# Performance work log

Hardware: AMD Instinct MI355X
Metric: run time of the kernel (lower is better)

## Reference

```python
import jax, jax.numpy as jnp
import numpy as np

N_ENT = 100000
N_USR = 50000
N_REL = 16
D = 64
E_KG = 1500000
E_CF = 1500000
N_LAYERS = 3
LEAKY_SLOPE = 0.01  # torch nn.LeakyReLU default


def setup_inputs() -> dict:
    key = jax.random.key(0)
    ks = jax.random.split(key, 14)
    inv = 1.0 / np.sqrt(D)
    return {
        "ent_user_embed": jax.random.normal(ks[0], (N_ENT + N_USR, D), jnp.float32) * inv,
        "rel_embed": jax.random.normal(ks[1], (N_REL, D), jnp.float32) * inv,
        "Wk_w": jax.random.normal(ks[2], (2 * D, D), jnp.float32) * (1.0 / np.sqrt(2 * D)),
        "Wk_b": jnp.zeros((D,), jnp.float32),
        "Wa_w": jax.random.normal(ks[3], (D, D), jnp.float32) * inv,
        "Wb_w": jax.random.normal(ks[4], (D, D), jnp.float32) * inv,
        "kg_h": jax.random.randint(ks[5], (E_KG,), 0, N_ENT, jnp.int32),
        "kg_t": jax.random.randint(ks[6], (E_KG,), 0, N_ENT, jnp.int32),
        "kg_r": jax.random.randint(ks[7], (E_KG,), 0, N_REL, jnp.int32),
        "ain_row": jax.random.randint(ks[8], (E_CF,), 0, N_ENT + N_USR, jnp.int32),
        "ain_col": jax.random.randint(ks[9], (E_CF,), 0, N_ENT + N_USR, jnp.int32),
        "ain_val": jax.random.uniform(ks[10], (E_CF,), jnp.float32) * (1.0 / 64.0),
        "user_ids": jax.random.randint(ks[11], (1024,), 0, N_USR, jnp.int32) + N_ENT,
        "item_ids": jax.random.randint(ks[12], (2048,), 0, N_ENT, jnp.int32),
        "n_entities": N_ENT,
        "n_users": N_USR,
    }


def reference(ent_user_embed, rel_embed, Wk_w, Wk_b, Wa_w, Wb_w,
              kg_h, kg_t, kg_r, ain_row, ain_col, ain_val,
              user_ids, item_ids, n_entities, n_users):
    # ---- update_attention: per-edge KG attention + sparse row-softmax ----
    h_e = ent_user_embed[kg_h]          # [E, D] gather
    t_e = ent_user_embed[kg_t]          # [E, D] gather
    r_e = rel_embed[kg_r]               # [E, D]
    trans = jnp.concatenate([t_e, h_e], axis=1) @ Wk_w + Wk_b  # W_k([t||h])
    logits = jnp.sum(trans * r_e, axis=1)                      # [E]
    logits = jnp.where(logits >= 0, logits, LEAKY_SLOPE * logits)
    row_max = jax.ops.segment_max(logits, kg_h, num_segments=n_entities)
    ex = jnp.exp(logits - row_max[kg_h])
    row_sum = jax.ops.segment_sum(ex, kg_h, num_segments=n_entities)
    attn = ex / row_sum[kg_h]           # sparse softmax over dim=1 (per head row)

    n_total = n_entities + n_users

    def spmm_kg(x):   # A_kg @ x, A_kg is [n_ent, n_ent] COO with attn values
        return jax.ops.segment_sum(attn[:, None] * x[kg_t], kg_h, num_segments=n_entities)

    def spmm_ain(x):  # A_in @ x, [n_total, n_total] COO
        return jax.ops.segment_sum(ain_val[:, None] * x[ain_col], ain_row, num_segments=n_total)

    def fusion_gate(kg_embed, ig_embed):
        g = jax.nn.sigmoid(kg_embed @ Wa_w + ig_embed @ Wb_w)
        return g * kg_embed + (1.0 - g) * ig_embed

    # ---- get_embeddings: L layers of dual propagation + gated fusion ----
    e_entities = ent_user_embed[:n_entities]
    e_users = ent_user_embed[n_entities:]
    user_sum = e_users
    item_sum = e_entities
    e_items_dual = e_entities
    e_users_curr = e_users
    e_entities_curr = e_entities
    for _ in range(N_LAYERS):
        e_items_kg = spmm_kg(e_entities_curr)
        ig_input = jnp.concatenate([e_items_dual, e_users_curr], axis=0)
        ig_output = spmm_ain(ig_input)
        e_items_collab = ig_output[:n_entities]
        e_users_new = ig_output[n_entities:]
        e_items_dual = fusion_gate(e_items_kg, e_items_collab)
        item_sum = item_sum + e_items_collab
        user_sum = user_sum + e_users_new
        e_users_curr = e_users_new
        e_entities_curr = e_items_kg
        # mess_dropout = [0,0,0] (eval mode): no-op
    all_embed = jnp.concatenate([item_sum, user_sum], axis=0)  # [n_total, D]

    # ---- calc_score ----
    return all_embed[user_ids] @ all_embed[item_ids].T  # [n_u, n_i]
```

## Files before the change

kernel.cpp:

```cpp
#include <hip/hip_runtime.h>
#include <math.h>

#define N_ENT 100000
#define N_USR 50000
#define N_TOT 150000
#define N_ROWS 250000
#define DD 64

#define SCAN_BLK 256
#define SCAN_ITEMS 1024

#define SORT_T 4096
#define BUK_SHIFT 8
#define NBUKU 977
#define LDSCAP 5120

typedef _Float16 half8 __attribute__((ext_vector_type(8)));
typedef _Float16 half4 __attribute__((ext_vector_type(4)));
typedef _Float16 h2v __attribute__((ext_vector_type(2)));
typedef float floatx4 __attribute__((ext_vector_type(4)));

__global__ void k_rel(const float* __restrict__ Wk_w, const float* __restrict__ Wk_b,
                      const float* __restrict__ rel, float* __restrict__ uvr) {
    int r = blockIdx.x;
    int k = threadIdx.x;
    const float* rv = rel + r * DD;
    const float* wrow = Wk_w + k * DD;
    float s = 0.f;
    for (int j = 0; j < DD; ++j) s += wrow[j] * rv[j];
    uvr[r * 132 + k] = s;
    if (k == 0) {
        float c = 0.f;
        for (int j = 0; j < DD; ++j) c += Wk_b[j] * rv[j];
        uvr[r * 132 + 128] = c;
    }
}

__global__ __launch_bounds__(256) void k_proj(const float* __restrict__ embed,
        const float* __restrict__ uvr, float* __restrict__ Puv) {
    __shared__ float suvr[64 * 32];
    for (int i = threadIdx.x; i < 64 * 32; i += 256) {
        int d = i >> 5, sub = i & 31;
        suvr[i] = uvr[(sub & 15) * 132 + (sub >> 4) * 64 + d];
    }
    __syncthreads();
    int rowi = threadIdx.x >> 5;
    int sub = threadIdx.x & 31;
    int row = blockIdx.x * 8 + rowi;
    if (row >= N_ENT) return;
    const float* er = embed + (size_t)row * DD;
    float s = 0.f;
    for (int d = 0; d < DD; ++d) s = fmaf(er[d], suvr[d * 32 + sub], s);
    Puv[(size_t)row * 32 + sub] = s;
}

__global__ __launch_bounds__(256) void k_sort_hist(const int* __restrict__ kg_h,
        const int* __restrict__ ain_row, int* __restrict__ tilecnt,
        int E_KG, int E_TOT, int NT) {
    __shared__ int hist[1024];
#pragma unroll
    for (int k = 0; k < 4; ++k) hist[k * 256 + threadIdx.x] = 0;
    __syncthreads();
    int tile = blockIdx.x;
    int base = tile * SORT_T;
#pragma unroll
    for (int k = 0; k < SORT_T / 256; ++k) {
        int e = base + k * 256 + threadIdx.x;
        if (e < E_TOT) {
            int row = (e < E_KG) ? kg_h[e] : (N_ENT + ain_row[e - E_KG]);
            atomicAdd(&hist[row >> BUK_SHIFT], 1);
        }
    }
    __syncthreads();
    for (int b = threadIdx.x; b < NBUKU; b += 256)
        tilecnt[b * NT + tile] = hist[b];
}

__global__ __launch_bounds__(SCAN_BLK) void k_blocksum(const int* __restrict__ cnt,
                                                       int* __restrict__ bsum, int n) {
    __shared__ int s[SCAN_BLK];
    int base = blockIdx.x * SCAN_ITEMS;
    int sum = 0;
    for (int i = threadIdx.x; i < SCAN_ITEMS; i += SCAN_BLK) {
        int idx = base + i;
        if (idx < n) sum += cnt[idx];
    }
    s[threadIdx.x] = sum;
    __syncthreads();
    for (int off = SCAN_BLK / 2; off; off >>= 1) {
        if (threadIdx.x < off) s[threadIdx.x] += s[threadIdx.x + off];
        __syncthreads();
    }
    if (threadIdx.x == 0) bsum[blockIdx.x] = s[0];
}

__global__ __launch_bounds__(1024) void k_bscan(int* __restrict__ bsum, int nb,
                                                int* __restrict__ total_out) {
    __shared__ int s[1024];
    int tid = threadIdx.x;
    int v = (tid < nb) ? bsum[tid] : 0;
    s[tid] = v;
    __syncthreads();
    for (int off = 1; off < 1024; off <<= 1) {
        int t = (tid >= off) ? s[tid - off] : 0;
        __syncthreads();
        s[tid] += t;
        __syncthreads();
    }
    if (tid < nb) bsum[tid] = s[tid] - v;
    if (tid == 1023) *total_out = s[1023];
}

__global__ __launch_bounds__(SCAN_BLK) void k_scan_apply(const int* __restrict__ cnt,
        int* __restrict__ scanned, const int* __restrict__ bsum, int n) {
    __shared__ int s[SCAN_BLK];
    int base = blockIdx.x * SCAN_ITEMS;
    int t = threadIdx.x;
    int idx0 = base + t * 4;
    int v[4];
    int lsum = 0;
#pragma unroll
    for (int k = 0; k < 4; ++k) {
        int idx = idx0 + k;
        v[k] = (idx < n) ? cnt[idx] : 0;
        lsum += v[k];
    }
    s[t] = lsum;
    __syncthreads();
    for (int off = 1; off < SCAN_BLK; off <<= 1) {
        int tv = (t >= off) ? s[t - off] : 0;
        __syncthreads();
        s[t] += tv;
        __syncthreads();
    }
    int pre = (t ? s[t - 1] : 0) + bsum[blockIdx.x];
#pragma unroll
    for (int k = 0; k < 4; ++k) {
        int idx = idx0 + k;
        if (idx < n) scanned[idx] = pre;
        pre += v[k];
    }
}

__global__ __launch_bounds__(256) void k_sort_scatter(const int* __restrict__ kg_h,
        const int* __restrict__ kg_t, const int* __restrict__ kg_r,
        const int* __restrict__ ain_row, const int* __restrict__ ain_col,
        const float* __restrict__ ain_val, const int* __restrict__ tilescan,
        int2* __restrict__ bufA, int E_KG, int E_TOT, int NT) {
    __shared__ int cur[1024];
    __shared__ int gbase[1024];
    int tid = threadIdx.x;
    int tile = blockIdx.x;
#pragma unroll
    for (int k = 0; k < 4; ++k) cur[k * 256 + tid] = 0;
    for (int b = tid; b < NBUKU; b += 256) gbase[b] = tilescan[b * NT + tile];
    __syncthreads();
    int base = tile * SORT_T;
#pragma unroll
    for (int k = 0; k < SORT_T / 256; ++k) {
        int e = base + k * 256 + tid;
        if (e < E_TOT) {
            int row, x, y;
            if (e < E_KG) {
                row = kg_h[e];
                x = kg_t[e] | (kg_r[e] << 17) | ((row & 255) << 22);
                y = 0;
            } else {
                int i = e - E_KG;
                row = N_ENT + ain_row[i];
                x = ain_col[i] | ((row & 255) << 22);
                y = __float_as_int(ain_val[i]);
            }
            int b = row >> BUK_SHIFT;
            int slot = atomicAdd(&cur[b], 1);
            bufA[gbase[b] + slot] = make_int2(x, y);
        }
    }
}

__global__ __launch_bounds__(256) void k_sort_fine(const int* __restrict__ tilescan,
        const int2* __restrict__ bufA, int2* __restrict__ pairbuf,
        int* __restrict__ rowptr, const float* __restrict__ Puv,
        const float* __restrict__ uvr, int NT) {
    __shared__ int2 seg[LDSCAP];
    __shared__ int rcnt[256];
    __shared__ int rexc[256];
    __shared__ int rcur[256];
    __shared__ float rsum[256];
    __shared__ float c16[16];
    int tid = threadIdx.x;
    int b = blockIdx.x;
    rcnt[tid] = 0;
    rsum[tid] = 0.f;
    if (tid < 16) c16[tid] = uvr[tid * 132 + 128];
    __syncthreads();

    int base = tilescan[b * NT];
    int endo = tilescan[(b + 1) * NT];
    int bsize = endo - base;
    int growbase = b << BUK_SHIFT;

    for (int i = base + tid; i < endo; i += 256) {
        unsigned rlow = ((unsigned)bufA[i].x) >> 22;
        atomicAdd(&rcnt[rlow], 1);
    }
    __syncthreads();

    {
        int v = rcnt[tid];
        rexc[tid] = v;
        __syncthreads();
        for (int off = 1; off < 256; off <<= 1) {
            int t = (tid >= off) ? rexc[tid - off] : 0;
            __syncthreads();
            rexc[tid] += t;
            __syncthreads();
        }
        int ex = rexc[tid] - v;
        rexc[tid] = ex;
        rcur[tid] = ex;
        int row = growbase + tid;
        if (row <= N_ROWS) rowptr[row] = base + ex;
    }
    __syncthreads();

    if (bsize <= LDSCAP) {
        for (int i = base + tid; i < endo; i += 256) {
            int2 p = bufA[i];
            unsigned rlow = ((unsigned)p.x) >> 22;
            seg[atomicAdd(&rcur[rlow], 1)] = p;
        }
        __syncthreads();
        for (int i = tid; i < bsize; i += 256) {
            int2 p = seg[i];
            unsigned rlow = ((unsigned)p.x) >> 22;
            int grow = growbase + (int)rlow;
            if (grow < N_ENT) {
                int t = p.x & 0x1FFFF;
                int r = (p.x >> 17) & 15;
                float lg = Puv[(size_t)t * 32 + r] + Puv[(size_t)grow * 32 + 16 + r] + c16[r];
                lg = lg >= 0.f ? lg : 0.01f * lg;
                float exv = expf(lg);
                seg[i].y = __float_as_int(exv);
                atomicAdd(&rsum[rlow], exv);
            }
        }
        __syncthreads();
        rsum[tid] = 1.f / rsum[tid];
        __syncthreads();
        for (int i = tid; i < bsize; i += 256) {
            int2 p = seg[i];
            unsigned rlow = ((unsigned)p.x) >> 22;
            if (growbase + (int)rlow < N_ENT)
                p.y = __float_as_int(__int_as_float(p.y) * rsum[rlow]);
            pairbuf[base + i] = p;
        }
    } else {
        for (int i = base + tid; i < endo; i += 256) {
            int2 p = bufA[i];
            unsigned rlow = ((unsigned)p.x) >> 22;
            int slot = atomicAdd(&rcur[rlow], 1);
            pairbuf[base + slot] = p;
        }
        __syncthreads();
        for (int i = base + tid; i < endo; i += 256) {
            int2 p = pairbuf[i];
            unsigned rlow = ((unsigned)p.x) >> 22;
            int grow = growbase + (int)rlow;
            if (grow < N_ENT) {
                int t = p.x & 0x1FFFF;
                int r = (p.x >> 17) & 15;
                float lg = Puv[(size_t)t * 32 + r] + Puv[(size_t)grow * 32 + 16 + r] + c16[r];
                lg = lg >= 0.f ? lg : 0.01f * lg;
                float exv = expf(lg);
                pairbuf[i].y = __float_as_int(exv);
                atomicAdd(&rsum[rlow], exv);
            }
        }
        __syncthreads();
        rsum[tid] = 1.f / rsum[tid];
        __syncthreads();
        for (int i = base + tid; i < endo; i += 256) {
            int2 p = pairbuf[i];
            unsigned rlow = ((unsigned)p.x) >> 22;
            if (growbase + (int)rlow < N_ENT)
                pairbuf[i].y = __float_as_int(__int_as_float(p.y) * rsum[rlow]);
        }
    }
}

__global__ void k_wcvt(const float* __restrict__ Wa, const float* __restrict__ Wb,
                       _Float16* __restrict__ wpack) {
    int i = blockIdx.x * 256 + threadIdx.x;
    if (i >= 8192) return;
    int m = i >> 12;
    int rem = i & 4095;
    int kstep = rem >> 11;
    int rem2 = rem & 2047;
    int ntile = rem2 >> 9;
    int rem3 = rem2 & 511;
    int lane = rem3 >> 3;
    int j = rem3 & 7;
    int k = kstep * 32 + (lane >> 4) * 8 + j;
    int n = ntile * 16 + (lane & 15);
    const float* W = m ? Wb : Wa;
    wpack[i] = (_Float16)W[k * 64 + n];
}

__global__ __launch_bounds__(256) void k_spmm_u(const int* __restrict__ rowptr,
        const int2* __restrict__ pairbuf, const _Float16* __restrict__ x,
        _Float16* __restrict__ outbuf, int row_begin, int row_end, int cmask) {
    int wid0 = (blockIdx.x * 256 + threadIdx.x) >> 6;
    int wpair = __builtin_amdgcn_readfirstlane(wid0);
    int lane = threadIdx.x & 63;
    int half = lane >> 5;
    int sub = lane & 31;
    int row = row_begin + wpair * 2 + half;
    if (row >= row_end) return;
    int d0 = sub * 2;
    const _Float16* xb = x + d0;
    int s = rowptr[row], e = rowptr[row + 1];
    float a00 = 0.f, a01 = 0.f, a10 = 0.f, a11 = 0.f;
    float a20 = 0.f, a21 = 0.f, a30 = 0.f, a31 = 0.f;
    int i = s;
    for (; i + 4 <= e; i += 4) {
        int2 p0 = pairbuf[i], p1 = pairbuf[i + 1], p2 = pairbuf[i + 2], p3 = pairbuf[i + 3];
        h2v g0 = *(const h2v*)(xb + (size_t)(p0.x & cmask) * DD);
        h2v g1 = *(const h2v*)(xb + (size_t)(p1.x & cmask) * DD);
        h2v g2 = *(const h2v*)(xb + (size_t)(p2.x & cmask) * DD);
        h2v g3 = *(const h2v*)(xb + (size_t)(p3.x & cmask) * DD);
        float w0 = __int_as_float(p0.y), w1 = __int_as_float(p1.y);
        float w2 = __int_as_float(p2.y), w3 = __int_as_float(p3.y);
        a00 = fmaf(w0, (float)g0[0], a00); a01 = fmaf(w0, (float)g0[1], a01);
        a10 = fmaf(w1, (float)g1[0], a10); a11 = fmaf(w1, (float)g1[1], a11);
        a20 = fmaf(w2, (float)g2[0], a20); a21 = fmaf(w2, (float)g2[1], a21);
        a30 = fmaf(w3, (float)g3[0], a30); a31 = fmaf(w3, (float)g3[1], a31);
    }
    for (; i < e; ++i) {
        int2 p = pairbuf[i];
        h2v g = *(const h2v*)(xb + (size_t)(p.x & cmask) * DD);
        float w = __int_as_float(p.y);
        a00 = fmaf(w, (float)g[0], a00); a01 = fmaf(w, (float)g[1], a01);
    }
    float r0 = (a00 + a10) + (a20 + a30);
    float r1 = (a01 + a11) + (a21 + a31);
    h2v st; st[0] = (_Float16)r0; st[1] = (_Float16)r1;
    *(h2v*)(outbuf + (size_t)(row - row_begin) * DD + d0) = st;
}

__global__ __launch_bounds__(256) void k_gate3(const _Float16* __restrict__ kg16,
        const _Float16* __restrict__ ig16, const _Float16* __restrict__ wpack,
        _Float16* __restrict__ dual16, int ngate) {
    __shared__ _Float16 sw[8192];
    if ((int)blockIdx.x >= ngate) {
        int i = ((int)blockIdx.x - ngate) * 256 + threadIdx.x;
        if (i < N_USR * DD / 8) {
            size_t o = (size_t)N_ENT * DD / 8 + i;
            ((half8*)dual16)[o] = ((const half8*)ig16)[o];
        }
        return;
    }
    for (int i = threadIdx.x * 8; i < 8192; i += 256 * 8)
        *(half8*)(sw + i) = *(const half8*)(wpack + i);
    __syncthreads();
    int lane = threadIdx.x & 63;
    int wv = (blockIdx.x * 256 + threadIdx.x) >> 6;
    int row0 = wv * 16;
    if (row0 >= N_ENT) return;
    int m = lane & 15;
    int quad = lane >> 4;

    const _Float16* kgr = kg16 + (size_t)(row0 + m) * DD + quad * 8;
    const _Float16* igr = ig16 + (size_t)(row0 + m) * DD + quad * 8;
    half8 akg0 = *(const half8*)(kgr);
    half8 akg1 = *(const half8*)(kgr + 32);
    half8 aig0 = *(const half8*)(igr);
    half8 aig1 = *(const half8*)(igr + 32);

    floatx4 acc[4];
#pragma unroll
    for (int t = 0; t < 4; ++t) {
        half8 bA0 = *(const half8*)(sw + 0 * 4096 + 0 * 2048 + t * 512 + lane * 8);
        half8 bA1 = *(const half8*)(sw + 0 * 4096 + 1 * 2048 + t * 512 + lane * 8);
        half8 bB0 = *(const half8*)(sw + 1 * 4096 + 0 * 2048 + t * 512 + lane * 8);
        half8 bB1 = *(const half8*)(sw + 1 * 4096 + 1 * 2048 + t * 512 + lane * 8);
        floatx4 c = {0.f, 0.f, 0.f, 0.f};
        c = __builtin_amdgcn_mfma_f32_16x16x32_f16(akg0, bA0, c, 0, 0, 0);
        c = __builtin_amdgcn_mfma_f32_16x16x32_f16(akg1, bA1, c, 0, 0, 0);
        c = __builtin_amdgcn_mfma_f32_16x16x32_f16(aig0, bB0, c, 0, 0, 0);
        c = __builtin_amdgcn_mfma_f32_16x16x32_f16(aig1, bB1, c, 0, 0, 0);
        acc[t] = c;
    }

#pragma unroll
    for (int t = 0; t < 4; ++t) {
#pragma unroll
        for (int r = 0; r < 4; ++r) {
            int row = quad * 4 + r;
            int col = t * 16 + m;
            size_t o = (size_t)(row0 + row) * DD + col;
            float kv = (float)kg16[o];
            float cv = (float)ig16[o];
            float g = 1.f / (1.f + expf(-acc[t][r]));
            dual16[o] = (_Float16)(g * kv + (1.f - g) * cv);
        }
    }
}

__global__ void k_init(const float* __restrict__ embed, _Float16* __restrict__ dual16) {
    int i = blockIdx.x * blockDim.x + threadIdx.x;
    if (i >= N_TOT * DD) return;
    dual16[i] = (_Float16)embed[i];
}

__global__ __launch_bounds__(256) void k_out(const float* __restrict__ embed,
        const _Float16* __restrict__ ig0, const _Float16* __restrict__ ig1,
        const _Float16* __restrict__ ig2, const int* __restrict__ user_ids,
        const int* __restrict__ item_ids, float* __restrict__ out) {
    __shared__ float uvec[32 * DD];
    int ug = blockIdx.x >> 3;
    int qi = blockIdx.x & 7;
    int ub = ug * 32;
    for (int i = threadIdx.x; i < 32 * DD; i += 256) {
        int uu = i >> 6, d = i & 63;
        size_t o = (size_t)user_ids[ub + uu] * DD + d;
        uvec[i] = embed[o] + (float)ig0[o] + (float)ig1[o] + (float)ig2[o];
    }
    __syncthreads();
    int jbase = qi * 256;
    for (int j = threadIdx.x; j < 256; j += 256) {
        size_t ro = (size_t)item_ids[jbase + j] * DD;
        float acc[32];
#pragma unroll
        for (int u = 0; u < 32; ++u) acc[u] = 0.f;
        for (int d = 0; d < DD; d += 4) {
            float4 ev = *(const float4*)(embed + ro + d);
            half4 h0 = *(const half4*)(ig0 + ro + d);
            half4 h1 = *(const half4*)(ig1 + ro + d);
            half4 h2 = *(const half4*)(ig2 + ro + d);
            float iv0 = ev.x + (float)h0[0] + (float)h1[0] + (float)h2[0];
            float iv1 = ev.y + (float)h0[1] + (float)h1[1] + (float)h2[1];
            float iv2 = ev.z + (float)h0[2] + (float)h1[2] + (float)h2[2];
            float iv3 = ev.w + (float)h0[3] + (float)h1[3] + (float)h2[3];
#pragma unroll
            for (int u = 0; u < 32; ++u) {
                acc[u] = fmaf(iv0, uvec[u * DD + d + 0], acc[u]);
                acc[u] = fmaf(iv1, uvec[u * DD + d + 1], acc[u]);
                acc[u] = fmaf(iv2, uvec[u * DD + d + 2], acc[u]);
                acc[u] = fmaf(iv3, uvec[u * DD + d + 3], acc[u]);
            }
        }
#pragma unroll
        for (int u = 0; u < 32; ++u)
            out[(size_t)(ub + u) * 2048 + jbase + j] = acc[u];
    }
}

extern "C" void kernel_launch(void* const* d_in, const int* in_sizes, int n_in,
                              void* d_out, int out_size, void* d_ws, size_t ws_size,
                              hipStream_t stream) {
    const float* embed   = (const float*)d_in[0];
    const float* rel     = (const float*)d_in[1];
    const float* Wk_w    = (const float*)d_in[2];
    const float* Wk_b    = (const float*)d_in[3];
    const float* Wa      = (const float*)d_in[4];
    const float* Wb      = (const float*)d_in[5];
    const int*   kg_h    = (const int*)d_in[6];
    const int*   kg_t    = (const int*)d_in[7];
    const int*   kg_r    = (const int*)d_in[8];
    const int*   ain_row = (const int*)d_in[9];
    const int*   ain_col = (const int*)d_in[10];
    const float* ain_val = (const float*)d_in[11];
    const int*   user_ids = (const int*)d_in[12];
    const int*   item_ids = (const int*)d_in[13];
    int E_KG = in_sizes[6];
    int E_CF = in_sizes[9];
    int E_TOT = E_KG + E_CF;
    float* out = (float*)d_out;

    int NT  = (E_TOT + SORT_T - 1) / SORT_T;
    int NTC = NBUKU * NT;

    float* ws = (float*)d_ws;
    size_t off = 0;
    float* uvr       = ws + off; off += 16 * 132;
    float* Puv       = ws + off; off += (size_t)N_ENT * 32;
    int*   rowptr    = (int*)(ws + off); off += N_ROWS + 4;
    int*   tilecnt   = (int*)(ws + off); off += (size_t)NTC + 4;
    int*   tilescan  = (int*)(ws + off); off += (size_t)NTC + 4;
    int*   bsum      = (int*)(ws + off); off += 1024;
    int2*  pairbuf   = (int2*)(ws + off); off += 2 * (size_t)E_TOT;
    _Float16* dual16 = (_Float16*)(ws + off); off += (size_t)N_TOT * DD / 2;
    _Float16* ig16_0 = (_Float16*)(ws + off); off += (size_t)N_TOT * DD / 2;
    _Float16* ig16_1 = (_Float16*)(ws + off); off += (size_t)N_TOT * DD / 2;
    _Float16* ig16_2 = (_Float16*)(ws + off); off += (size_t)N_TOT * DD / 2;
    _Float16* kg16A  = (_Float16*)(ws + off); off += (size_t)N_ENT * DD / 2;
    _Float16* kg16B  = (_Float16*)(ws + off); off += (size_t)N_ENT * DD / 2;
    _Float16* wpack  = (_Float16*)(ws + off); off += 8192 / 2;
    int2*  bufA      = (int2*)kg16A;
    _Float16* ig_l[3] = {ig16_0, ig16_1, ig16_2};

    hipLaunchKernelGGL(k_rel, dim3(16), dim3(128), 0, stream, Wk_w, Wk_b, rel, uvr);
    hipLaunchKernelGGL(k_proj, dim3((N_ENT + 7) / 8), dim3(256), 0, stream, embed, uvr, Puv);

    hipLaunchKernelGGL(k_sort_hist, dim3(NT), dim3(256), 0, stream,
                       kg_h, ain_row, tilecnt, E_KG, E_TOT, NT);
    int nb = (NTC + SCAN_ITEMS - 1) / SCAN_ITEMS;
    hipLaunchKernelGGL(k_blocksum, dim3(nb), dim3(SCAN_BLK), 0, stream, tilecnt, bsum, NTC);
    hipLaunchKernelGGL(k_bscan, dim3(1), dim3(1024), 0, stream, bsum, nb, tilescan + NTC);
    hipLaunchKernelGGL(k_scan_apply, dim3(nb), dim3(SCAN_BLK), 0, stream,
                       tilecnt, tilescan, bsum, NTC);
    hipLaunchKernelGGL(k_sort_scatter, dim3(NT), dim3(256), 0, stream,
                       kg_h, kg_t, kg_r, ain_row, ain_col, ain_val, tilescan,
                       bufA, E_KG, E_TOT, NT);
    hipLaunchKernelGGL(k_sort_fine, dim3(NBUKU), dim3(256), 0, stream,
                       tilescan, bufA, pairbuf, rowptr, Puv, uvr, NT);

    hipLaunchKernelGGL(k_init, dim3((N_TOT * DD + 255) / 256), dim3(256), 0, stream,
                       embed, dual16);
    hipLaunchKernelGGL(k_wcvt, dim3(32), dim3(256), 0, stream, Wa, Wb, wpack);

    const _Float16* cur16 = dual16;
    _Float16* kg16o = kg16A;
    _Float16* kg16alt = kg16B;
    int kg_blocks = ((N_ENT / 2) * 64 + 255) / 256;
    int cf_blocks = ((N_TOT / 2) * 64 + 255) / 256;
    int ngate = (N_ENT / 16 + 3) / 4;
    int nuc = (N_USR * DD / 8 + 255) / 256;
    for (int layer = 0; layer < 3; ++layer) {
        if (layer < 2) {
            hipLaunchKernelGGL(k_spmm_u, dim3(kg_blocks), dim3(256), 0, stream,
                               rowptr, pairbuf, cur16, kg16o, 0, N_ENT, 0x1FFFF);
            hipLaunchKernelGGL(k_spmm_u, dim3(cf_blocks), dim3(256), 0, stream,
                               rowptr, pairbuf, dual16, ig_l[layer], N_ENT, N_ROWS, 0x3FFFF);
            hipLaunchKernelGGL(k_gate3, dim3(ngate + nuc), dim3(256), 0, stream,
                               kg16o, ig_l[layer], wpack, dual16, ngate);
            cur16 = kg16o;
            kg16o = kg16alt;
            kg16alt = (_Float16*)cur16;
        } else {
            hipLaunchKernelGGL(k_spmm_u, dim3(cf_blocks), dim3(256), 0, stream,
                               rowptr, pairbuf, dual16, ig_l[layer], N_ENT, N_ROWS, 0x3FFFF);
        }
    }

    hipLaunchKernelGGL(k_out, dim3(256), dim3(256), 0, stream,
                       embed, ig16_0, ig16_1, ig16_2, user_ids, item_ids, out);
}
```

Before: 647.2 us.

## Stage bucket scatter through LDS for coalesced global writes in sort

```diff
diff --git a/kernel.cpp b/kernel.cpp
--- a/kernel.cpp
+++ b/kernel.cpp
@@ -147,20 +147,26 @@
         const int* __restrict__ ain_row, const int* __restrict__ ain_col,
         const float* __restrict__ ain_val, const int* __restrict__ tilescan,
         int2* __restrict__ bufA, int E_KG, int E_TOT, int NT) {
+    __shared__ int2 seg[SORT_T];
+    __shared__ short sbuk[SORT_T];
+    __shared__ int hist[1024];
     __shared__ int cur[1024];
-    __shared__ int gbase[1024];
+    __shared__ int ssum[256];
     int tid = threadIdx.x;
     int tile = blockIdx.x;
 #pragma unroll
-    for (int k = 0; k < 4; ++k) cur[k * 256 + tid] = 0;
-    for (int b = tid; b < NBUKU; b += 256) gbase[b] = tilescan[b * NT + tile];
-    __syncthreads();
+    for (int k = 0; k < 4; ++k) hist[k * 256 + tid] = 0;
+    __syncthreads();
+
     int base = tile * SORT_T;
+    int px[SORT_T / 256], py[SORT_T / 256];
+    short pb[SORT_T / 256];
 #pragma unroll
     for (int k = 0; k < SORT_T / 256; ++k) {
         int e = base + k * 256 + tid;
+        int x = 0, y = 0, b = -1;
         if (e < E_TOT) {
-            int row, x, y;
+            int row;
             if (e < E_KG) {
                 row = kg_h[e];
                 x = kg_t[e] | (kg_r[e] << 17) | ((row & 255) << 22);
@@ -171,10 +177,51 @@
                 x = ain_col[i] | ((row & 255) << 22);
                 y = __float_as_int(ain_val[i]);
             }
-            int b = row >> BUK_SHIFT;
-            int slot = atomicAdd(&cur[b], 1);
-            bufA[gbase[b] + slot] = make_int2(x, y);
-        }
+            b = row >> BUK_SHIFT;
+            atomicAdd(&hist[b], 1);
+        }
+        px[k] = x; py[k] = y; pb[k] = (short)b;
+    }
+    __syncthreads();
+
+    {
+        int b0 = 4 * tid;
+        int v0 = hist[b0], v1 = hist[b0 + 1], v2 = hist[b0 + 2], v3 = hist[b0 + 3];
+        int g0 = (b0     < NBUKU) ? tilescan[(b0    ) * NT + tile] : 0;
+        int g1 = (b0 + 1 < NBUKU) ? tilescan[(b0 + 1) * NT + tile] : 0;
+        int g2 = (b0 + 2 < NBUKU) ? tilescan[(b0 + 2) * NT + tile] : 0;
+        int g3 = (b0 + 3 < NBUKU) ? tilescan[(b0 + 3) * NT + tile] : 0;
+        int lsum = v0 + v1 + v2 + v3;
+        ssum[tid] = lsum;
+        __syncthreads();
+        for (int off = 1; off < 256; off <<= 1) {
+            int t = (tid >= off) ? ssum[tid - off] : 0;
+            __syncthreads();
+            ssum[tid] += t;
+            __syncthreads();
+        }
+        int ex = ssum[tid] - lsum;
+        cur[b0] = ex;     hist[b0] = g0 - ex;     ex += v0;
+        cur[b0 + 1] = ex; hist[b0 + 1] = g1 - ex; ex += v1;
+        cur[b0 + 2] = ex; hist[b0 + 2] = g2 - ex; ex += v2;
+        cur[b0 + 3] = ex; hist[b0 + 3] = g3 - ex;
+    }
+    __syncthreads();
+
+#pragma unroll
+    for (int k = 0; k < SORT_T / 256; ++k) {
+        if (pb[k] >= 0) {
+            int slot = atomicAdd(&cur[pb[k]], 1);
+            seg[slot] = make_int2(px[k], py[k]);
+            sbuk[slot] = pb[k];
+        }
+    }
+    __syncthreads();
+
+    int cnt = min(SORT_T, E_TOT - base);
+    for (int i = tid; i < cnt; i += 256) {
+        int b = sbuk[i];
+        bufA[hist[b] + i] = seg[i];
     }
 }
 
```

After: 603.0 us. -6.8%, faster.
